# Optimization experiments

Measured on AMD Instinct MI355X. Metric: run time of the kernel, lower is better.

## Reference

```python
import jax, jax.numpy as jnp
import numpy as np
import math

N_HEADS = 16
EMBED = 1024
D_HEAD = EMBED // N_HEADS
B, L = 2, 2048


def setup_inputs() -> dict:
    key = jax.random.key(0)
    k1, k2, k3, k4, k5 = jax.random.split(key, 5)
    s = 0.02
    return {
        "x": jax.random.normal(k1, (B, L, EMBED), dtype=jnp.float32),
        "w_qkv": jax.random.normal(k2, (3 * EMBED, EMBED), dtype=jnp.float32) * s,
        "b_qkv": jax.random.normal(k3, (3 * EMBED,), dtype=jnp.float32) * s,
        "w_out": jax.random.normal(k4, (EMBED, EMBED), dtype=jnp.float32) * s,
        "b_out": jax.random.normal(k5, (EMBED,), dtype=jnp.float32) * s,
        "mask": 1,
    }


def reference(x, w_qkv, b_qkv, w_out, b_out, mask):
    b, l, e = x.shape
    qkv = x @ w_qkv.T + b_qkv                      # (B, L, 3E)
    q, k, v = jnp.split(qkv, 3, axis=-1)
    # (B, L, H, d) -> (B, H, L, d)
    q = q.reshape(b, l, N_HEADS, D_HEAD).transpose(0, 2, 1, 3)
    k = k.reshape(b, l, N_HEADS, D_HEAD).transpose(0, 2, 1, 3)
    v = v.reshape(b, l, N_HEADS, D_HEAD).transpose(0, 2, 1, 3)
    # NOTE: faithful to source bug -- scores use V, not K
    scores = jnp.einsum("bhld,bhmd->bhlm", q, v) * (1.0 / math.sqrt(D_HEAD))
    if mask:
        causal = jnp.triu(jnp.ones((l, l), dtype=bool), k=1)  # (L, L)
        scores = jnp.where(causal, -jnp.inf, scores)
    attn = jax.nn.softmax(scores, axis=-1)          # (B, H, L, L)
    out = jnp.einsum("bhlm,bhmd->bhld", attn, v)    # (B, H, L, d)
    # NOTE: faithful to source bug -- transpose(1,2) result discarded,
    # so reshape straight from (B, H, L, d) to (B, L, E)
    out = out.reshape(b, l, e)
    return out @ w_out.T + b_out
```

## Files before the change

kernel.cpp:

```cpp
#include <hip/hip_runtime.h>
#include <math.h>

constexpr int Lc = 2048, Ec = 1024, Hc = 16, Dc = 64;

typedef __attribute__((ext_vector_type(8))) short bf16x8;
typedef __attribute__((ext_vector_type(4))) float f32x4;
typedef unsigned short u16;
typedef unsigned int u32;

#define MFMA16(a, b, c) __builtin_amdgcn_mfma_f32_16x16x32_bf16(a, b, c, 0, 0, 0)

__device__ inline u16 f2bf(float f) {
  u32 u = __builtin_bit_cast(u32, f);
  u32 r = u + 0x7fff + ((u >> 16) & 1);
  return (u16)(r >> 16);
}

__device__ inline void gld16(const void* g, void* l) {
  __builtin_amdgcn_global_load_lds(
      (const __attribute__((address_space(1))) u32*)g,
      (__attribute__((address_space(3))) u32*)l, 16, 0, 0);
}

constexpr size_t XN = (size_t)4096 * 1024;
constexpr size_t WQN = (size_t)2048 * 1024;
constexpr size_t WON = (size_t)1024 * 1024;

__global__ __launch_bounds__(256) void convert_all(
    const float* __restrict__ x, const float* __restrict__ wqkv,
    const float* __restrict__ wout, u16* __restrict__ xb,
    u16* __restrict__ wqb, u16* __restrict__ wob)
{
  const size_t i = ((size_t)blockIdx.x * 256 + threadIdx.x) * 4;
  float4 v;
  u16* dst;
  if (i < XN) {
    v = *(const float4*)(x + i);
    dst = xb + i;
  } else if (i < XN + WQN) {
    const size_t off = i - XN;
    const size_t row = off >> 10, col = off & 1023;
    const size_t srow = row + ((row >> 10) << 10);
    v = *(const float4*)(wqkv + srow * 1024 + col);
    dst = wqb + off;
  } else {
    const size_t off = i - XN - WQN;
    v = *(const float4*)(wout + off);
    dst = wob + off;
  }
  u16 o0 = f2bf(v.x), o1 = f2bf(v.y), o2 = f2bf(v.z), o3 = f2bf(v.w);
  dst[0] = o0; dst[1] = o1; dst[2] = o2; dst[3] = o3;
}

__global__ __launch_bounds__(256) void transpose_v(
    const u16* __restrict__ V, u16* __restrict__ Vt)
{
  __shared__ __align__(16) u16 T[64][72];
  const int bh = blockIdx.y, lt = blockIdx.x * 64;
  const int r = threadIdx.x >> 2;
  const int c = (threadIdx.x & 3) * 16;
  const u16* src = V + ((size_t)bh * Lc + lt) * Dc;
  *(bf16x8*)&T[r][c]     = *(const bf16x8*)(src + (size_t)r * 64 + c);
  *(bf16x8*)&T[r][c + 8] = *(const bf16x8*)(src + (size_t)r * 64 + c + 8);
  __syncthreads();
  bf16x8 o0, o1;
#pragma unroll
  for (int j = 0; j < 8; ++j) o0[j] = (short)T[c + j][r];
#pragma unroll
  for (int j = 0; j < 8; ++j) o1[j] = (short)T[c + 8 + j][r];
  u16* dst = Vt + ((size_t)bh * Dc + r) * Lc + lt + c;
  *(bf16x8*)dst = o0;
  *(bf16x8*)(dst + 8) = o1;
}

__global__ __launch_bounds__(256) void gemm_qv(
    const u16* __restrict__ A, const u16* __restrict__ W,
    const float* __restrict__ bqkv, u16* __restrict__ Q, u16* __restrict__ V)
{
  __shared__ __align__(16) u16 As[2][4096];
  __shared__ __align__(16) u16 Bs[2][4096];
  const int tid = threadIdx.x;
  const int w = tid >> 6, lane = tid & 63;
  const int quad = lane >> 4, l16 = lane & 15;
  const int wm = w >> 1, wn = w & 1;
  const int rowTile = blockIdx.y * 128;
  const int colTile = blockIdx.x * 128;

  const int r0 = tid >> 2, o0 = (tid & 3) * 8;
  const u16* Ab0 = A + (size_t)(rowTile + r0) * 1024 + o0;
  const u16* Ab1 = Ab0 + (size_t)64 * 1024;
  const u16* Bb0 = W + (size_t)(colTile + r0) * 1024 + o0;
  const u16* Bb1 = Bb0 + (size_t)64 * 1024;

  f32x4 acc[4][4] = {};

  gld16(Ab0, &As[0][tid * 8]);
  gld16(Ab1, &As[0][2048 + tid * 8]);
  gld16(Bb0, &Bs[0][tid * 8]);
  gld16(Bb1, &Bs[0][2048 + tid * 8]);

  int cur = 0;
  for (int k0 = 0; k0 < 1024; k0 += 32) {
    __syncthreads();
    if (k0 + 32 < 1024) {
      const int sb = cur ^ 1, kn = k0 + 32;
      gld16(Ab0 + kn, &As[sb][tid * 8]);
      gld16(Ab1 + kn, &As[sb][2048 + tid * 8]);
      gld16(Bb0 + kn, &Bs[sb][tid * 8]);
      gld16(Bb1 + kn, &Bs[sb][2048 + tid * 8]);
    }
    bf16x8 af[4], bf[4];
#pragma unroll
    for (int s = 0; s < 4; ++s)
      af[s] = *(const bf16x8*)&As[cur][(wm * 64 + s * 16 + l16) * 32 + quad * 8];
#pragma unroll
    for (int n = 0; n < 4; ++n)
      bf[n] = *(const bf16x8*)&Bs[cur][(wn * 64 + n * 16 + l16) * 32 + quad * 8];
#pragma unroll
    for (int s = 0; s < 4; ++s)
#pragma unroll
      for (int n = 0; n < 4; ++n)
        acc[s][n] = MFMA16(af[s], bf[n], acc[s][n]);
    cur ^= 1;
  }

#pragma unroll
  for (int n = 0; n < 4; ++n) {
    const int gn = colTile + wn * 64 + n * 16 + l16;
    const bool isV = gn >= 1024;
    const float bias = bqkv[gn + (isV ? 1024 : 0)];
    const float scl = isV ? 1.0f : 0.125f;
    const int h = (gn & 1023) >> 6, d = gn & 63;
    u16* dst = isV ? V : Q;
#pragma unroll
    for (int s = 0; s < 4; ++s) {
#pragma unroll
      for (int r = 0; r < 4; ++r) {
        const int gm = rowTile + wm * 64 + s * 16 + quad * 4 + r;
        const int b = gm >> 11, l = gm & 2047;
        dst[(((size_t)(b * Hc + h)) * Lc + l) * Dc + d] = f2bf((acc[s][n][r] + bias) * scl);
      }
    }
  }
}

constexpr int PSTR = 72;

__global__ __launch_bounds__(256) void attn_mfma(
    const u16* __restrict__ Q, const u16* __restrict__ V,
    const u16* __restrict__ Vt, u16* __restrict__ outA)
{
  __shared__ __align__(16) u16 lds[2 * 4096 + 2 * 4096 + 4 * 16 * PSTR];
  const int tid = threadIdx.x;
  const int w = tid >> 6, lane = tid & 63;
  const int quad = lane >> 4, l16 = lane & 15;
  const int bh = blockIdx.y;
  const int b = bh >> 4, h = bh & 15;
  const u16* Qb = Q + (size_t)bh * Lc * Dc;
  const u16* Vb = V + (size_t)bh * Lc * Dc;
  const u16* Vtb = Vt + (size_t)bh * Dc * Lc;
  u16* Ps = &lds[16384 + w * 16 * PSTR];

  const int b1 = tid * 16, b2 = b1 + 4096;
  const int e1 = (b1 ^ (((b1 >> 7) & 7) << 4)) >> 1;
  const int e2 = (b2 ^ (((b2 >> 7) & 7) << 4)) >> 1;
  const u16* vs1 = Vb + e1;
  const u16* vs2 = Vb + e2;
  const u16* ts1 = Vtb + (size_t)(e1 >> 6) * Lc + (e1 & 63);
  const u16* ts2 = Vtb + (size_t)(e2 >> 6) * Lc + (e2 & 63);

  int roff[4][2];
#pragma unroll
  for (int i = 0; i < 4; ++i)
#pragma unroll
    for (int kk = 0; kk < 2; ++kk) {
      const int byte = ((i * 16 + l16) << 7) + kk * 64 + quad * 16;
      roff[i][kk] = (byte ^ ((l16 & 7) << 4)) >> 1;
    }

  for (int half = 0; half < 2; ++half) {
    const int qt = half ? (31 - blockIdx.x) : blockIdx.x;
    const int q0 = qt * 64;
    const int nt = qt + 1;
    const int wqmin = q0 + w * 16;

    bf16x8 qf[2];
#pragma unroll
    for (int kk = 0; kk < 2; ++kk)
      qf[kk] = *(const bf16x8*)(Qb + (size_t)(q0 + w * 16 + l16) * 64 + kk * 32 + quad * 8);

    f32x4 O[4] = {};
    float lsum[4] = {0.f, 0.f, 0.f, 0.f};

    __syncthreads();
    gld16(vs1, &lds[tid * 8]);
    gld16(vs2, &lds[2048 + tid * 8]);
    gld16(ts1, &lds[8192 + tid * 8]);
    gld16(ts2, &lds[8192 + 2048 + tid * 8]);

    int cur = 0;
    for (int t = 0; t < nt; ++t) {
      const int kt = t * 64;
      __syncthreads();
      if (t + 1 < nt) {
        const int sb = cur ^ 1, nk = kt + 64;
        gld16(vs1 + (size_t)nk * 64, &lds[sb * 4096 + tid * 8]);
        gld16(vs2 + (size_t)nk * 64, &lds[sb * 4096 + 2048 + tid * 8]);
        gld16(ts1 + nk, &lds[8192 + sb * 4096 + tid * 8]);
        gld16(ts2 + nk, &lds[8192 + sb * 4096 + 2048 + tid * 8]);
      }
      if (kt <= wqmin + 15) {
        const u16* VsB = &lds[cur * 4096];
        const u16* VtB = &lds[8192 + cur * 4096];

        f32x4 sf[4] = {};
#pragma unroll
        for (int nb = 0; nb < 4; ++nb) {
          sf[nb] = MFMA16(qf[0], *(const bf16x8*)(VsB + roff[nb][0]), sf[nb]);
          sf[nb] = MFMA16(qf[1], *(const bf16x8*)(VsB + roff[nb][1]), sf[nb]);
        }

        const bool needmask = (kt + 63 > wqmin);
#pragma unroll
        for (int nb = 0; nb < 4; ++nb)
#pragma unroll
          for (int r = 0; r < 4; ++r) {
            float p = __expf(sf[nb][r]);
            if (needmask) {
              const int key = kt + nb * 16 + l16;
              const int qr = wqmin + quad * 4 + r;
              if (key > qr) p = 0.f;
            }
            lsum[r] += p;
            Ps[(quad * 4 + r) * PSTR + nb * 16 + l16] = f2bf(p);
          }

        bf16x8 pf[2];
#pragma unroll
        for (int kk = 0; kk < 2; ++kk)
          pf[kk] = *(const bf16x8*)&Ps[l16 * PSTR + kk * 32 + quad * 8];
#pragma unroll
        for (int db = 0; db < 4; ++db) {
          O[db] = MFMA16(pf[0], *(const bf16x8*)(VtB + roff[db][0]), O[db]);
          O[db] = MFMA16(pf[1], *(const bf16x8*)(VtB + roff[db][1]), O[db]);
        }
      }
      cur ^= 1;
    }

#pragma unroll
    for (int r = 0; r < 4; ++r) {
      float l = lsum[r];
      l += __shfl_xor(l, 1);
      l += __shfl_xor(l, 2);
      l += __shfl_xor(l, 4);
      l += __shfl_xor(l, 8);
      const float inv = 1.f / l;
      const int q = q0 + w * 16 + quad * 4 + r;
      const int orow = h * 128 + (q >> 4);
      const int cbase = (q & 15) << 6;
#pragma unroll
      for (int db = 0; db < 4; ++db)
        outA[((size_t)b * Lc + orow) * Ec + cbase + db * 16 + l16] =
            f2bf(O[db][r] * inv);
    }
  }
}

__global__ __launch_bounds__(256) void gemm_out(
    const u16* __restrict__ A, const u16* __restrict__ W,
    const float* __restrict__ bias, float* __restrict__ out)
{
  __shared__ __align__(16) u16 As[2][4096];
  __shared__ __align__(16) u16 Bs[2][4096];
  const int tid = threadIdx.x;
  const int w = tid >> 6, lane = tid & 63;
  const int quad = lane >> 4, l16 = lane & 15;
  const int wm = w >> 1, wn = w & 1;
  const int rowTile = blockIdx.y * 128;
  const int colTile = blockIdx.x * 128;

  const int r0 = tid >> 2, o0 = (tid & 3) * 8;
  const u16* Ab0 = A + (size_t)(rowTile + r0) * 1024 + o0;
  const u16* Ab1 = Ab0 + (size_t)64 * 1024;
  const u16* Bb0 = W + (size_t)(colTile + r0) * 1024 + o0;
  const u16* Bb1 = Bb0 + (size_t)64 * 1024;

  f32x4 acc[4][4] = {};

  gld16(Ab0, &As[0][tid * 8]);
  gld16(Ab1, &As[0][2048 + tid * 8]);
  gld16(Bb0, &Bs[0][tid * 8]);
  gld16(Bb1, &Bs[0][2048 + tid * 8]);

  int cur = 0;
  for (int k0 = 0; k0 < 1024; k0 += 32) {
    __syncthreads();
    if (k0 + 32 < 1024) {
      const int sb = cur ^ 1, kn = k0 + 32;
      gld16(Ab0 + kn, &As[sb][tid * 8]);
      gld16(Ab1 + kn, &As[sb][2048 + tid * 8]);
      gld16(Bb0 + kn, &Bs[sb][tid * 8]);
      gld16(Bb1 + kn, &Bs[sb][2048 + tid * 8]);
    }
    bf16x8 af[4], bf[4];
#pragma unroll
    for (int s = 0; s < 4; ++s)
      af[s] = *(const bf16x8*)&As[cur][(wm * 64 + s * 16 + l16) * 32 + quad * 8];
#pragma unroll
    for (int n = 0; n < 4; ++n)
      bf[n] = *(const bf16x8*)&Bs[cur][(wn * 64 + n * 16 + l16) * 32 + quad * 8];
#pragma unroll
    for (int s = 0; s < 4; ++s)
#pragma unroll
      for (int n = 0; n < 4; ++n)
        acc[s][n] = MFMA16(af[s], bf[n], acc[s][n]);
    cur ^= 1;
  }

#pragma unroll
  for (int n = 0; n < 4; ++n) {
    const int gn = colTile + wn * 64 + n * 16 + l16;
    const float bn = bias[gn];
#pragma unroll
    for (int s = 0; s < 4; ++s)
#pragma unroll
      for (int r = 0; r < 4; ++r) {
        const int gm = rowTile + wm * 64 + s * 16 + quad * 4 + r;
        out[(size_t)gm * 1024 + gn] = acc[s][n][r] + bn;
      }
  }
}

extern "C" void kernel_launch(void* const* d_in, const int* in_sizes, int n_in,
                              void* d_out, int out_size, void* d_ws, size_t ws_size,
                              hipStream_t stream) {
  (void)in_sizes; (void)n_in; (void)out_size; (void)ws_size;
  const float* x     = (const float*)d_in[0];
  const float* w_qkv = (const float*)d_in[1];
  const float* b_qkv = (const float*)d_in[2];
  const float* w_out = (const float*)d_in[3];
  const float* b_out = (const float*)d_in[4];
  float* out = (float*)d_out;

  u16* xb  = (u16*)d_ws;
  u16* wqb = xb + XN;
  u16* wob = wqb + WQN;
  u16* Qw  = wob + WON;
  u16* Vw  = Qw + (size_t)2 * Hc * Lc * Dc;
  u16* Vtw = Vw + (size_t)2 * Hc * Lc * Dc;
  u16* Aw  = Vtw + (size_t)2 * Hc * Lc * Dc;

  convert_all<<<7168, 256, 0, stream>>>(x, w_qkv, w_out, xb, wqb, wob);
  gemm_qv<<<dim3(16, 32), 256, 0, stream>>>(xb, wqb, b_qkv, Qw, Vw);
  transpose_v<<<dim3(32, 32), 256, 0, stream>>>(Vw, Vtw);
  attn_mfma<<<dim3(16, 32), 256, 0, stream>>>(Qw, Vw, Vtw, Aw);
  gemm_out<<<dim3(8, 32), 256, 0, stream>>>(Aw, wob, b_out, out);
}
```

Before: 179.8 us.

## Fuse paired causal query tiles into one KV sweep and remap blocks per XCD

Each block now processes its low and high query tiles together in a single pass over the V/Vt key tiles, so the shared key tiles are loaded once and fed to both tiles. Before, each tile had its own sweep. The V fragments are read from LDS into registers once per step, and the P scratch is doubled. The launch grid is flattened to 1D and remapped so that blocks of the same heads land on the same XCD, for better L2 locality. Costs are more registers from two accumulators and the preloaded fragments, plus more LDS, which may lower occupancy.

New measurement: 176.1 us. -2.1%, faster.

```diff
diff --git a/kernel.cpp b/kernel.cpp
--- a/kernel.cpp
+++ b/kernel.cpp
@@ -146,20 +146,61 @@
 
 constexpr int PSTR = 72;
 
+__device__ inline void attn_half(
+    const bf16x8 qf[2], const bf16x8 bv[4][2], const bf16x8 bvt[4][2],
+    u16* __restrict__ Ps, f32x4 O[4], float lsum[4],
+    int kt, int wq, bool needmask, int quad, int l16)
+{
+  f32x4 sf[4] = {};
+#pragma unroll
+  for (int nb = 0; nb < 4; ++nb) {
+    sf[nb] = MFMA16(qf[0], bv[nb][0], sf[nb]);
+    sf[nb] = MFMA16(qf[1], bv[nb][1], sf[nb]);
+  }
+#pragma unroll
+  for (int nb = 0; nb < 4; ++nb)
+#pragma unroll
+    for (int r = 0; r < 4; ++r) {
+      float p = __expf(sf[nb][r]);
+      if (needmask) {
+        const int key = kt + nb * 16 + l16;
+        const int qr = wq + quad * 4 + r;
+        if (key > qr) p = 0.f;
+      }
+      lsum[r] += p;
+      Ps[(quad * 4 + r) * PSTR + nb * 16 + l16] = f2bf(p);
+    }
+  bf16x8 pf[2];
+#pragma unroll
+  for (int kk = 0; kk < 2; ++kk)
+    pf[kk] = *(const bf16x8*)&Ps[l16 * PSTR + kk * 32 + quad * 8];
+#pragma unroll
+  for (int db = 0; db < 4; ++db) {
+    O[db] = MFMA16(pf[0], bvt[db][0], O[db]);
+    O[db] = MFMA16(pf[1], bvt[db][1], O[db]);
+  }
+}
+
 __global__ __launch_bounds__(256) void attn_mfma(
     const u16* __restrict__ Q, const u16* __restrict__ V,
     const u16* __restrict__ Vt, u16* __restrict__ outA)
 {
-  __shared__ __align__(16) u16 lds[2 * 4096 + 2 * 4096 + 4 * 16 * PSTR];
+  __shared__ __align__(16) u16 lds[2 * 4096 + 2 * 4096 + 2 * 4 * 16 * PSTR];
   const int tid = threadIdx.x;
   const int w = tid >> 6, lane = tid & 63;
   const int quad = lane >> 4, l16 = lane & 15;
-  const int bh = blockIdx.y;
+
+  const int flat = blockIdx.x;
+  const int xcd = flat & 7, slot = flat >> 3;
+  const int bh = xcd * 4 + (slot >> 4);
+  const int xblk = slot & 15;
   const int b = bh >> 4, h = bh & 15;
+
   const u16* Qb = Q + (size_t)bh * Lc * Dc;
   const u16* Vb = V + (size_t)bh * Lc * Dc;
   const u16* Vtb = Vt + (size_t)bh * Dc * Lc;
-  u16* Ps = &lds[16384 + w * 16 * PSTR];
+  u16* Psl = &lds[16384 + w * 16 * PSTR];
+  u16* Psh = &lds[16384 + (4 + w) * 16 * PSTR];
 
   const int b1 = tid * 16, b2 = b1 + 4096;
   const int e1 = (b1 ^ (((b1 >> 7) & 7) << 4)) >> 1;
@@ -178,79 +219,63 @@
       roff[i][kk] = (byte ^ ((l16 & 7) << 4)) >> 1;
     }
 
+  const int qlo = xblk, qhi = 31 - xblk;
+  const int nt = qhi + 1;
+  const int wqlo = qlo * 64 + w * 16;
+  const int wqhi = qhi * 64 + w * 16;
+
+  bf16x8 qfl[2], qfh[2];
+#pragma unroll
+  for (int kk = 0; kk < 2; ++kk) {
+    qfl[kk] = *(const bf16x8*)(Qb + (size_t)(qlo * 64 + w * 16 + l16) * 64 + kk * 32 + quad * 8);
+    qfh[kk] = *(const bf16x8*)(Qb + (size_t)(qhi * 64 + w * 16 + l16) * 64 + kk * 32 + quad * 8);
+  }
+
+  f32x4 Ol[4] = {}, Oh[4] = {};
+  float lsl[4] = {0.f, 0.f, 0.f, 0.f}, lsh[4] = {0.f, 0.f, 0.f, 0.f};
+
+  gld16(vs1, &lds[tid * 8]);
+  gld16(vs2, &lds[2048 + tid * 8]);
+  gld16(ts1, &lds[8192 + tid * 8]);
+  gld16(ts2, &lds[8192 + 2048 + tid * 8]);
+
+  int cur = 0;
+  for (int t = 0; t < nt; ++t) {
+    const int kt = t * 64;
+    __syncthreads();
+    if (t + 1 < nt) {
+      const int sb = cur ^ 1, nk = kt + 64;
+      gld16(vs1 + (size_t)nk * 64, &lds[sb * 4096 + tid * 8]);
+      gld16(vs2 + (size_t)nk * 64, &lds[sb * 4096 + 2048 + tid * 8]);
+      gld16(ts1 + nk, &lds[8192 + sb * 4096 + tid * 8]);
+      gld16(ts2 + nk, &lds[8192 + sb * 4096 + 2048 + tid * 8]);
+    }
+    const u16* VsB = &lds[cur * 4096];
+    const u16* VtB = &lds[8192 + cur * 4096];
+
+    bf16x8 bv[4][2], bvt[4][2];
+#pragma unroll
+    for (int nb = 0; nb < 4; ++nb)
+#pragma unroll
+      for (int kk = 0; kk < 2; ++kk) {
+        bv[nb][kk] = *(const bf16x8*)(VsB + roff[nb][kk]);
+        bvt[nb][kk] = *(const bf16x8*)(VtB + roff[nb][kk]);
+      }
+
+    attn_half(qfh, bv, bvt, Psh, Oh, lsh, kt, wqhi, t == qhi, quad, l16);
+    if (t <= qlo)
+      attn_half(qfl, bv, bvt, Psl, Ol, lsl, kt, wqlo, t == qlo, quad, l16);
+    cur ^= 1;
+  }
+
+#pragma unroll
   for (int half = 0; half < 2; ++half) {
-    const int qt = half ? (31 - blockIdx.x) : blockIdx.x;
-    const int q0 = qt * 64;
-    const int nt = qt + 1;
-    const int wqmin = q0 + w * 16;
-
-    bf16x8 qf[2];
-#pragma unroll
-    for (int kk = 0; kk < 2; ++kk)
-      qf[kk] = *(const bf16x8*)(Qb + (size_t)(q0 + w * 16 + l16) * 64 + kk * 32 + quad * 8);
-
-    f32x4 O[4] = {};
-    float lsum[4] = {0.f, 0.f, 0.f, 0.f};
-
-    __syncthreads();
-    gld16(vs1, &lds[tid * 8]);
-    gld16(vs2, &lds[2048 + tid * 8]);
-    gld16(ts1, &lds[8192 + tid * 8]);
-    gld16(ts2, &lds[8192 + 2048 + tid * 8]);
-
-    int cur = 0;
-    for (int t = 0; t < nt; ++t) {
-      const int kt = t * 64;
-      __syncthreads();
-      if (t + 1 < nt) {
-        const int sb = cur ^ 1, nk = kt + 64;
-        gld16(vs1 + (size_t)nk * 64, &lds[sb * 4096 + tid * 8]);
-        gld16(vs2 + (size_t)nk * 64, &lds[sb * 4096 + 2048 + tid * 8]);
-        gld16(ts1 + nk, &lds[8192 + sb * 4096 + tid * 8]);
-        gld16(ts2 + nk, &lds[8192 + sb * 4096 + 2048 + tid * 8]);
-      }
-      if (kt <= wqmin + 15) {
-        const u16* VsB = &lds[cur * 4096];
-        const u16* VtB = &lds[8192 + cur * 4096];
-
-        f32x4 sf[4] = {};
-#pragma unroll
-        for (int nb = 0; nb < 4; ++nb) {
-          sf[nb] = MFMA16(qf[0], *(const bf16x8*)(VsB + roff[nb][0]), sf[nb]);
-          sf[nb] = MFMA16(qf[1], *(const bf16x8*)(VsB + roff[nb][1]), sf[nb]);
-        }
-
-        const bool needmask = (kt + 63 > wqmin);
-#pragma unroll
-        for (int nb = 0; nb < 4; ++nb)
-#pragma unroll
-          for (int r = 0; r < 4; ++r) {
-            float p = __expf(sf[nb][r]);
-            if (needmask) {
-              const int key = kt + nb * 16 + l16;
-              const int qr = wqmin + quad * 4 + r;
-              if (key > qr) p = 0.f;
-            }
-            lsum[r] += p;
-            Ps[(quad * 4 + r) * PSTR + nb * 16 + l16] = f2bf(p);
-          }
-
-        bf16x8 pf[2];
-#pragma unroll
-        for (int kk = 0; kk < 2; ++kk)
-          pf[kk] = *(const bf16x8*)&Ps[l16 * PSTR + kk * 32 + quad * 8];
-#pragma unroll
-        for (int db = 0; db < 4; ++db) {
-          O[db] = MFMA16(pf[0], *(const bf16x8*)(VtB + roff[db][0]), O[db]);
-          O[db] = MFMA16(pf[1], *(const bf16x8*)(VtB + roff[db][1]), O[db]);
-        }
-      }
-      cur ^= 1;
-    }
-
+    const int q0 = half ? qhi * 64 : qlo * 64;
+    const f32x4* O = half ? Oh : Ol;
+    const float* ls = half ? lsh : lsl;
 #pragma unroll
     for (int r = 0; r < 4; ++r) {
-      float l = lsum[r];
+      float l = ls[r];
       l += __shfl_xor(l, 1);
       l += __shfl_xor(l, 2);
       l += __shfl_xor(l, 4);
@@ -354,6 +379,6 @@
   convert_all<<<7168, 256, 0, stream>>>(x, w_qkv, w_out, xb, wqb, wob);
   gemm_qv<<<dim3(16, 32), 256, 0, stream>>>(xb, wqb, b_qkv, Qw, Vw);
   transpose_v<<<dim3(32, 32), 256, 0, stream>>>(Vw, Vtw);
-  attn_mfma<<<dim3(16, 32), 256, 0, stream>>>(Qw, Vw, Vtw, Aw);
+  attn_mfma<<<512, 256, 0, stream>>>(Qw, Vw, Vtw, Aw);
   gemm_out<<<dim3(8, 32), 256, 0, stream>>>(Aw, wob, b_out, out);
 }
```

## Use 128-row query tiles per block with XCD-aware head mapping in attention

Applied to the files above, without the earlier changes.

Each attention block now handles 128 query rows (32 per wave, in two 16-row sub-tiles), up from two 64-row tiles processed in turn. Each V and V-transpose fragment loaded from LDS is reused across both sub-tiles, halving LDS reads per MFMA. The grid is flattened to 512 blocks. Heads are mapped so that blocks on the same XCD share a batch-head, and the largest causal tiles are scheduled first. The cost is more registers for the doubled accumulators and coarser load balancing across causal tiles of different length.

New measurement: 192.2 us. +6.9%, slower.

```diff
diff --git a/kernel.cpp b/kernel.cpp
--- a/kernel.cpp
+++ b/kernel.cpp
@@ -150,16 +150,25 @@
     const u16* __restrict__ Q, const u16* __restrict__ V,
     const u16* __restrict__ Vt, u16* __restrict__ outA)
 {
-  __shared__ __align__(16) u16 lds[2 * 4096 + 2 * 4096 + 4 * 16 * PSTR];
+  __shared__ __align__(16) u16 lds[25600];
   const int tid = threadIdx.x;
   const int w = tid >> 6, lane = tid & 63;
   const int quad = lane >> 4, l16 = lane & 15;
-  const int bh = blockIdx.y;
+
+  const int flat = blockIdx.x;
+  const int xcd = flat & 7, slot = flat >> 3;
+  const int bh = xcd * 4 + (slot & 3);
+  const int p = 15 - (slot >> 2);
   const int b = bh >> 4, h = bh & 15;
+
+  const int q0 = p * 128;
+  const int nt = 2 * p + 2;
+  const int wq = q0 + w * 32;
+
   const u16* Qb = Q + (size_t)bh * Lc * Dc;
   const u16* Vb = V + (size_t)bh * Lc * Dc;
   const u16* Vtb = Vt + (size_t)bh * Dc * Lc;
-  u16* Ps = &lds[16384 + w * 16 * PSTR];
+  u16* Ps = &lds[16384 + w * 32 * PSTR];
 
   const int b1 = tid * 16, b2 = b1 + 4096;
   const int e1 = (b1 ^ (((b1 >> 7) & 7) << 4)) >> 1;
@@ -178,91 +187,107 @@
       roff[i][kk] = (byte ^ ((l16 & 7) << 4)) >> 1;
     }
 
-  for (int half = 0; half < 2; ++half) {
-    const int qt = half ? (31 - blockIdx.x) : blockIdx.x;
-    const int q0 = qt * 64;
-    const int nt = qt + 1;
-    const int wqmin = q0 + w * 16;
-
-    bf16x8 qf[2];
+  bf16x8 qf[2][2];
+#pragma unroll
+  for (int s = 0; s < 2; ++s)
 #pragma unroll
     for (int kk = 0; kk < 2; ++kk)
-      qf[kk] = *(const bf16x8*)(Qb + (size_t)(q0 + w * 16 + l16) * 64 + kk * 32 + quad * 8);
-
-    f32x4 O[4] = {};
-    float lsum[4] = {0.f, 0.f, 0.f, 0.f};
-
+      qf[s][kk] = *(const bf16x8*)(Qb + (size_t)(wq + s * 16 + l16) * 64 + kk * 32 + quad * 8);
+
+  f32x4 O[2][4] = {};
+  float lsum[2][4] = {{0.f, 0.f, 0.f, 0.f}, {0.f, 0.f, 0.f, 0.f}};
+
+  gld16(vs1, &lds[tid * 8]);
+  gld16(vs2, &lds[2048 + tid * 8]);
+  gld16(ts1, &lds[8192 + tid * 8]);
+  gld16(ts2, &lds[8192 + 2048 + tid * 8]);
+
+  int cur = 0;
+  for (int t = 0; t < nt; ++t) {
+    const int kt = t * 64;
     __syncthreads();
-    gld16(vs1, &lds[tid * 8]);
-    gld16(vs2, &lds[2048 + tid * 8]);
-    gld16(ts1, &lds[8192 + tid * 8]);
-    gld16(ts2, &lds[8192 + 2048 + tid * 8]);
-
-    int cur = 0;
-    for (int t = 0; t < nt; ++t) {
-      const int kt = t * 64;
-      __syncthreads();
-      if (t + 1 < nt) {
-        const int sb = cur ^ 1, nk = kt + 64;
-        gld16(vs1 + (size_t)nk * 64, &lds[sb * 4096 + tid * 8]);
-        gld16(vs2 + (size_t)nk * 64, &lds[sb * 4096 + 2048 + tid * 8]);
-        gld16(ts1 + nk, &lds[8192 + sb * 4096 + tid * 8]);
-        gld16(ts2 + nk, &lds[8192 + sb * 4096 + 2048 + tid * 8]);
-      }
-      if (kt <= wqmin + 15) {
-        const u16* VsB = &lds[cur * 4096];
-        const u16* VtB = &lds[8192 + cur * 4096];
-
+    if (t + 1 < nt) {
+      const int sb = cur ^ 1, nk = kt + 64;
+      gld16(vs1 + (size_t)nk * 64, &lds[sb * 4096 + tid * 8]);
+      gld16(vs2 + (size_t)nk * 64, &lds[sb * 4096 + 2048 + tid * 8]);
+      gld16(ts1 + nk, &lds[8192 + sb * 4096 + tid * 8]);
+      gld16(ts2 + nk, &lds[8192 + sb * 4096 + 2048 + tid * 8]);
+    }
+    if (kt <= wq + 31) {
+      const u16* VsB = &lds[cur * 4096];
+      const u16* VtB = &lds[8192 + cur * 4096];
+
+      bf16x8 bv[4][2];
+#pragma unroll
+      for (int nb = 0; nb < 4; ++nb)
+#pragma unroll
+        for (int kk = 0; kk < 2; ++kk)
+          bv[nb][kk] = *(const bf16x8*)(VsB + roff[nb][kk]);
+
+#pragma unroll
+      for (int s = 0; s < 2; ++s) {
         f32x4 sf[4] = {};
 #pragma unroll
         for (int nb = 0; nb < 4; ++nb) {
-          sf[nb] = MFMA16(qf[0], *(const bf16x8*)(VsB + roff[nb][0]), sf[nb]);
-          sf[nb] = MFMA16(qf[1], *(const bf16x8*)(VsB + roff[nb][1]), sf[nb]);
+          sf[nb] = MFMA16(qf[s][0], bv[nb][0], sf[nb]);
+          sf[nb] = MFMA16(qf[s][1], bv[nb][1], sf[nb]);
         }
-
-        const bool needmask = (kt + 63 > wqmin);
+        const bool needmask = (kt + 63 > wq + s * 16);
 #pragma unroll
         for (int nb = 0; nb < 4; ++nb)
 #pragma unroll
           for (int r = 0; r < 4; ++r) {
-            float p = __expf(sf[nb][r]);
+            float pv = __expf(sf[nb][r]);
             if (needmask) {
               const int key = kt + nb * 16 + l16;
-              const int qr = wqmin + quad * 4 + r;
-              if (key > qr) p = 0.f;
+              const int qr = wq + s * 16 + quad * 4 + r;
+              if (key > qr) pv = 0.f;
             }
-            lsum[r] += p;
-            Ps[(quad * 4 + r) * PSTR + nb * 16 + l16] = f2bf(p);
+            lsum[s][r] += pv;
+            Ps[(s * 16 + quad * 4 + r) * PSTR + nb * 16 + l16] = f2bf(pv);
           }
-
+      }
+
+      bf16x8 bvt[4][2];
+#pragma unroll
+      for (int db = 0; db < 4; ++db)
+#pragma unroll
+        for (int kk = 0; kk < 2; ++kk)
+          bvt[db][kk] = *(const bf16x8*)(VtB + roff[db][kk]);
+
+#pragma unroll
+      for (int s = 0; s < 2; ++s) {
         bf16x8 pf[2];
 #pragma unroll
         for (int kk = 0; kk < 2; ++kk)
-          pf[kk] = *(const bf16x8*)&Ps[l16 * PSTR + kk * 32 + quad * 8];
+          pf[kk] = *(const bf16x8*)&Ps[(s * 16 + l16) * PSTR + kk * 32 + quad * 8];
 #pragma unroll
         for (int db = 0; db < 4; ++db) {
-          O[db] = MFMA16(pf[0], *(const bf16x8*)(VtB + roff[db][0]), O[db]);
-          O[db] = MFMA16(pf[1], *(const bf16x8*)(VtB + roff[db][1]), O[db]);
+          O[s][db] = MFMA16(pf[0], bvt[db][0], O[s][db]);
+          O[s][db] = MFMA16(pf[1], bvt[db][1], O[s][db]);
         }
       }
-      cur ^= 1;
-    }
-
+    }
+    cur ^= 1;
+  }
+
+#pragma unroll
+  for (int s = 0; s < 2; ++s) {
 #pragma unroll
     for (int r = 0; r < 4; ++r) {
-      float l = lsum[r];
+      float l = lsum[s][r];
       l += __shfl_xor(l, 1);
       l += __shfl_xor(l, 2);
       l += __shfl_xor(l, 4);
       l += __shfl_xor(l, 8);
       const float inv = 1.f / l;
-      const int q = q0 + w * 16 + quad * 4 + r;
+      const int q = wq + s * 16 + quad * 4 + r;
       const int orow = h * 128 + (q >> 4);
       const int cbase = (q & 15) << 6;
 #pragma unroll
       for (int db = 0; db < 4; ++db)
         outA[((size_t)b * Lc + orow) * Ec + cbase + db * 16 + l16] =
-            f2bf(O[db][r] * inv);
+            f2bf(O[s][db][r] * inv);
     }
   }
 }
@@ -354,6 +379,6 @@
   convert_all<<<7168, 256, 0, stream>>>(x, w_qkv, w_out, xb, wqb, wob);
   gemm_qv<<<dim3(16, 32), 256, 0, stream>>>(xb, wqb, b_qkv, Qw, Vw);
   transpose_v<<<dim3(32, 32), 256, 0, stream>>>(Vw, Vtw);
-  attn_mfma<<<dim3(16, 32), 256, 0, stream>>>(Qw, Vw, Vtw, Aw);
+  attn_mfma<<<512, 256, 0, stream>>>(Qw, Vw, Vtw, Aw);
   gemm_out<<<dim3(8, 32), 256, 0, stream>>>(Aw, wob, b_out, out);
 }
```
